# Kernel tuning notes

Hardware: AMD Instinct MI355X
Metric: run time of the kernel (lower is better)

The kernel has to match this reference:

```python
import jax, jax.numpy as jnp
import numpy as np

B, H, W = 32, 56, 56
C_IN, C_OUT, GROUPS, K = 256, 256, 32, 3
EPS = 1e-5


def setup_inputs() -> dict:
    key = jax.random.key(0)
    k1, k2 = jax.random.split(key, 2)
    x = jax.random.normal(k1, (B, H, W, C_IN), dtype=jnp.float32)
    # HWIO grouped-conv kernel: I = C_IN // GROUPS = 8; equivalent to the
    # concatenation of the 32 per-group [3,3,8,8] Conv2d kernels along O.
    w = jax.random.normal(k2, (K, K, C_IN // GROUPS, C_OUT), dtype=jnp.float32) * 0.05
    b = jnp.zeros((C_OUT,), dtype=jnp.float32)
    gamma = jnp.ones((C_OUT,), dtype=jnp.float32)
    beta = jnp.zeros((C_OUT,), dtype=jnp.float32)
    return {"x": x, "w": w, "b": b, "gamma": gamma, "beta": beta}


def reference(x, w, b, gamma, beta):
    # Grouped conv: same math as tf.split -> per-group Conv2d -> tf.concat,
    # expressed as one native grouped convolution (feature_group_count).
    y = jax.lax.conv_general_dilated(
        x, w,
        window_strides=(1, 1),
        padding="SAME",
        dimension_numbers=("NHWC", "HWIO", "NHWC"),
        feature_group_count=GROUPS,
    ) + b  # [B,H,W,C_OUT]
    # BatchNorm (training forward: batch statistics over N,H,W per channel)
    mean = jnp.mean(y, axis=(0, 1, 2))
    var = jnp.var(y, axis=(0, 1, 2))
    y = (y - mean) * jax.lax.rsqrt(var + EPS) * gamma + beta
    # Act('relu')
    return jax.nn.relu(y)
```

## Files before the change

kernel.cpp:

```cpp
#include <hip/hip_runtime.h>
#include <hip/hip_bf16.h>

#define BB 32
#define HH 56
#define WW 56
#define CC 256
#define NPIX (BB*HH*WW)
#define EPS 1e-5f

typedef short bf16x8 __attribute__((ext_vector_type(8)));
typedef float f32x4  __attribute__((ext_vector_type(4)));

__device__ __forceinline__ unsigned short f2bf(float f) {
    __hip_bfloat16 h = __float2bfloat16(f);
    return *reinterpret_cast<unsigned short*>(&h);
}


__global__ void k0_zero(float* stats) { stats[threadIdx.x] = 0.f; }

__global__ __launch_bounds__(256) void k1_conv(
    const float* __restrict__ x, const float* __restrict__ wgt,
    __hip_bfloat16* __restrict__ y, float* __restrict__ stats)
{
    __shared__ unsigned short xt[10*58*24];
    __shared__ unsigned short wb[16*160];
    __shared__ float bsum[16], bsq[16];

    const int gp = blockIdx.x;
    const int hb = blockIdx.y;
    const int b  = blockIdx.z;
    const int t  = threadIdx.x;
    const int h0 = hb * 8;

    if (t < 16) { bsum[t] = 0.f; bsq[t] = 0.f; }

    float4 v[10];
    int    off[10];
    #pragma unroll
    for (int j = 0; j < 10; ++j) {
        const int i   = j*256 + t;
        const int ci4 = i & 3;
        const int cq  = i >> 2;
        const int row = cq / 58;
        const int col = cq - row*58;
        const int hh  = h0 - 1 + row;
        const int wc  = col - 1;
        off[j] = (row*58 + col)*24 + ci4*4;
        v[j] = make_float4(0.f, 0.f, 0.f, 0.f);
        if (i < 2320 && (unsigned)hh < HH && (unsigned)wc < WW)
            v[j] = *(const float4*)(x + (((size_t)(b*HH + hh)*WW + wc)*CC + gp*16 + ci4*4));
    }
    {
        const int n  = t >> 4;
        const int k0 = t & 15;
        #pragma unroll
        for (int j = 0; j < 10; ++j) {
            const int kk  = k0 + j*16;
            const int g   = (kk >= 80);
            const int r   = kk - g*80;
            const int tap = r >> 3, ci = r & 7;
            unsigned short val = 0;
            if (tap < 9 && (n >> 3) == g)
                val = f2bf(wgt[(tap*8 + ci)*CC + gp*16 + n]);
            wb[n*160 + kk] = val;
        }
    }
    #pragma unroll
    for (int j = 0; j < 10; ++j) {
        if (j*256 + t < 2320) {
            ushort4 s;
            s.x = f2bf(v[j].x); s.y = f2bf(v[j].y);
            s.z = f2bf(v[j].z); s.w = f2bf(v[j].w);
            *(ushort4*)(xt + off[j]) = s;
        }
    }
    __syncthreads();

    const int lane = t & 63;
    const int rp   = t >> 6;
    const int n    = lane & 15;
    const int q    = lane >> 4;
    const int m    = lane & 15;
    const int rowr = rp*2 + (m >> 3);
    const int colb = m & 7;

    bf16x8 bfrag[5];
    #pragma unroll
    for (int s = 0; s < 5; ++s)
        bfrag[s] = *(const bf16x8*)(wb + n*160 + s*32 + q*8);

    int aoff[5];
    #pragma unroll
    for (int s = 0; s < 5; ++s) {
        int o  = s*4 + q;
        int g  = (o >= 10);
        int tp = o - g*10;
        if (tp == 9) tp = 0;
        int dh = tp / 3, dw = tp - dh*3;
        aoff[s] = ((rowr + dh)*58 + colb + dw)*24 + g*8;
    }

    const int hq = q >> 1;
    const int wq = (q & 1) * 4;
    float lsum = 0.f, lsq = 0.f;

    #pragma unroll 2
    for (int ct = 0; ct < 7; ++ct) {
        f32x4 acc = {0.f, 0.f, 0.f, 0.f};
        #pragma unroll
        for (int s = 0; s < 5; ++s) {
            bf16x8 af = *(const bf16x8*)(xt + aoff[s] + ct*192);
            acc = __builtin_amdgcn_mfma_f32_16x16x32_bf16(af, bfrag[s], acc, 0, 0, 0);
        }
        const int h = h0 + rp*2 + hq;
        const size_t base = (((size_t)(b*HH + h))*WW + ct*8 + wq)*CC + gp*16 + n;
        #pragma unroll
        for (int i = 0; i < 4; ++i) {
            float vv = acc[i];
            y[base + (size_t)i*CC] = __float2bfloat16(vv);
            lsum += vv;
            lsq  += vv * vv;
        }
    }

    atomicAdd(&bsum[n], lsum);
    atomicAdd(&bsq[n],  lsq);
    __syncthreads();
    if (t < 16) {
        atomicAdd(&stats[gp*16 + t],       bsum[t]);
        atomicAdd(&stats[256 + gp*16 + t], bsq[t]);
    }
}

__global__ void k2_finalize(const float* __restrict__ stats,
                            const float* __restrict__ gamma,
                            const float* __restrict__ beta,
                            float* __restrict__ ss)
{
    int c = threadIdx.x;
    float inv_n = 1.f / (float)NPIX;
    float mean = stats[c] * inv_n;
    float var  = stats[256 + c] * inv_n - mean * mean;
    float scale = gamma[c] * rsqrtf(var + EPS);
    ss[c]       = scale;
    ss[256 + c] = beta[c] - mean * scale;
}

__global__ __launch_bounds__(256) void k3_norm(
    const __hip_bfloat16* __restrict__ y, const float* __restrict__ ss,
    float* __restrict__ out)
{
    const int t   = threadIdx.x;
    const int oct = t & 31;
    const int pr  = t >> 5;
    const int c0  = oct * 8;

    float4 sc0 = *(const float4*)(ss + c0);
    float4 sc1 = *(const float4*)(ss + c0 + 4);
    float4 sh0 = *(const float4*)(ss + 256 + c0);
    float4 sh1 = *(const float4*)(ss + 256 + c0 + 4);

    const uint4* yv = (const uint4*)y;
    float4* ov = (float4*)out;
    const int px0 = blockIdx.x * 32 + pr;

    uint4 d[4];
    #pragma unroll
    for (int i = 0; i < 4; ++i)
        d[i] = yv[(size_t)(px0 + i*8)*32 + oct];

    #pragma unroll
    for (int i = 0; i < 4; ++i) {
        const int px = px0 + i*8;
        float f0 = __uint_as_float((d[i].x & 0xffffu) << 16);
        float f1 = __uint_as_float(d[i].x & 0xffff0000u);
        float f2 = __uint_as_float((d[i].y & 0xffffu) << 16);
        float f3 = __uint_as_float(d[i].y & 0xffff0000u);
        float f4 = __uint_as_float((d[i].z & 0xffffu) << 16);
        float f5 = __uint_as_float(d[i].z & 0xffff0000u);
        float f6 = __uint_as_float((d[i].w & 0xffffu) << 16);
        float f7 = __uint_as_float(d[i].w & 0xffff0000u);

        float4 o0, o1;
        o0.x = fmaxf(0.f, f0 * sc0.x + sh0.x);
        o0.y = fmaxf(0.f, f1 * sc0.y + sh0.y);
        o0.z = fmaxf(0.f, f2 * sc0.z + sh0.z);
        o0.w = fmaxf(0.f, f3 * sc0.w + sh0.w);
        o1.x = fmaxf(0.f, f4 * sc1.x + sh1.x);
        o1.y = fmaxf(0.f, f5 * sc1.y + sh1.y);
        o1.z = fmaxf(0.f, f6 * sc1.z + sh1.z);
        o1.w = fmaxf(0.f, f7 * sc1.w + sh1.w);

        ov[(size_t)px*64 + oct*2]     = o0;
        ov[(size_t)px*64 + oct*2 + 1] = o1;
    }
}

extern "C" void kernel_launch(void* const* d_in, const int* in_sizes, int n_in,
                              void* d_out, int out_size, void* d_ws, size_t ws_size,
                              hipStream_t stream) {
    const float* x     = (const float*)d_in[0];
    const float* wgt   = (const float*)d_in[1];
    const float* gamma = (const float*)d_in[3];
    const float* beta  = (const float*)d_in[4];
    float* out = (float*)d_out;

    float* stats = (float*)d_ws;
    float* ss    = (float*)((char*)d_ws + 2048);
    __hip_bfloat16* y = (__hip_bfloat16*)((char*)d_ws + 4096);

    k0_zero<<<1, 512, 0, stream>>>(stats);
    k1_conv<<<dim3(16, 7, BB), 256, 0, stream>>>(x, wgt, y, stats);
    k2_finalize<<<1, 256, 0, stream>>>(stats, gamma, beta, ss);
    k3_norm<<<NPIX/32, 256, 0, stream>>>(y, ss, out);
}
```

Measured before the change: 253.9 us.

## Swap MFMA operands for vectorized bf16 stores and load weights directly to registers

Swaps the A/B operands of the MFMA so each lane's accumulator holds 4 consecutive output channels for one pixel. This allows one 8-byte vector store of bf16 results instead of four scattered 2-byte stores. Weight fragments are now loaded directly from global memory into registers, which removes the shared weight buffer and its staging. Per-channel statistics are reduced with wavefront shuffles before a few LDS atomics, replacing per-lane LDS atomics, and launch bounds request 5 blocks per SM.

```diff
diff --git a/kernel.cpp b/kernel.cpp
--- a/kernel.cpp
+++ b/kernel.cpp
@@ -19,12 +19,11 @@
 
 __global__ void k0_zero(float* stats) { stats[threadIdx.x] = 0.f; }
 
-__global__ __launch_bounds__(256) void k1_conv(
+__global__ __launch_bounds__(256, 5) void k1_conv(
     const float* __restrict__ x, const float* __restrict__ wgt,
     __hip_bfloat16* __restrict__ y, float* __restrict__ stats)
 {
     __shared__ unsigned short xt[10*58*24];
-    __shared__ unsigned short wb[16*160];
     __shared__ float bsum[16], bsq[16];
 
     const int gp = blockIdx.x;
@@ -51,21 +50,6 @@
         if (i < 2320 && (unsigned)hh < HH && (unsigned)wc < WW)
             v[j] = *(const float4*)(x + (((size_t)(b*HH + hh)*WW + wc)*CC + gp*16 + ci4*4));
     }
-    {
-        const int n  = t >> 4;
-        const int k0 = t & 15;
-        #pragma unroll
-        for (int j = 0; j < 10; ++j) {
-            const int kk  = k0 + j*16;
-            const int g   = (kk >= 80);
-            const int r   = kk - g*80;
-            const int tap = r >> 3, ci = r & 7;
-            unsigned short val = 0;
-            if (tap < 9 && (n >> 3) == g)
-                val = f2bf(wgt[(tap*8 + ci)*CC + gp*16 + n]);
-            wb[n*160 + kk] = val;
-        }
-    }
     #pragma unroll
     for (int j = 0; j < 10; ++j) {
         if (j*256 + t < 2320) {
@@ -75,20 +59,32 @@
             *(ushort4*)(xt + off[j]) = s;
         }
     }
-    __syncthreads();
 
     const int lane = t & 63;
     const int rp   = t >> 6;
     const int n    = lane & 15;
     const int q    = lane >> 4;
+
+    bf16x8 wfrag[5];
+    #pragma unroll
+    for (int s = 0; s < 5; ++s) {
+        const int o   = s*4 + q;
+        const int g   = (o >= 10);
+        const int tap = o - g*10;
+        bf16x8 f = {0,0,0,0,0,0,0,0};
+        if (tap < 9 && (n >> 3) == g) {
+            #pragma unroll
+            for (int e = 0; e < 8; ++e)
+                f[e] = (short)f2bf(wgt[(tap*8 + e)*CC + gp*16 + n]);
+        }
+        wfrag[s] = f;
+    }
+
+    __syncthreads();
+
     const int m    = lane & 15;
     const int rowr = rp*2 + (m >> 3);
     const int colb = m & 7;
-
-    bf16x8 bfrag[5];
-    #pragma unroll
-    for (int s = 0; s < 5; ++s)
-        bfrag[s] = *(const bf16x8*)(wb + n*160 + s*32 + q*8);
 
     int aoff[5];
     #pragma unroll
@@ -101,9 +97,10 @@
         aoff[s] = ((rowr + dh)*58 + colb + dw)*24 + g*8;
     }
 
-    const int hq = q >> 1;
-    const int wq = (q & 1) * 4;
-    float lsum = 0.f, lsq = 0.f;
+    const int h = h0 + rowr;
+    const size_t pixbase = ((size_t)(b*HH + h))*WW;
+    float lsum[4] = {0.f, 0.f, 0.f, 0.f};
+    float lsq[4]  = {0.f, 0.f, 0.f, 0.f};
 
     #pragma unroll 2
     for (int ct = 0; ct < 7; ++ct) {
@@ -111,21 +108,34 @@
         #pragma unroll
         for (int s = 0; s < 5; ++s) {
             bf16x8 af = *(const bf16x8*)(xt + aoff[s] + ct*192);
-            acc = __builtin_amdgcn_mfma_f32_16x16x32_bf16(af, bfrag[s], acc, 0, 0, 0);
-        }
-        const int h = h0 + rp*2 + hq;
-        const size_t base = (((size_t)(b*HH + h))*WW + ct*8 + wq)*CC + gp*16 + n;
+            acc = __builtin_amdgcn_mfma_f32_16x16x32_bf16(wfrag[s], af, acc, 0, 0, 0);
+        }
+        ushort4 st;
+        st.x = f2bf(acc[0]); st.y = f2bf(acc[1]);
+        st.z = f2bf(acc[2]); st.w = f2bf(acc[3]);
+        *(ushort4*)(y + (pixbase + ct*8 + colb)*CC + gp*16 + q*4) = st;
         #pragma unroll
         for (int i = 0; i < 4; ++i) {
-            float vv = acc[i];
-            y[base + (size_t)i*CC] = __float2bfloat16(vv);
-            lsum += vv;
-            lsq  += vv * vv;
-        }
-    }
-
-    atomicAdd(&bsum[n], lsum);
-    atomicAdd(&bsq[n],  lsq);
+            lsum[i] += acc[i];
+            lsq[i]  += acc[i]*acc[i];
+        }
+    }
+
+    #pragma unroll
+    for (int d = 8; d >= 1; d >>= 1) {
+        #pragma unroll
+        for (int i = 0; i < 4; ++i) {
+            lsum[i] += __shfl_xor(lsum[i], d);
+            lsq[i]  += __shfl_xor(lsq[i],  d);
+        }
+    }
+    if (m == 0) {
+        #pragma unroll
+        for (int i = 0; i < 4; ++i) {
+            atomicAdd(&bsum[q*4 + i], lsum[i]);
+            atomicAdd(&bsq[q*4 + i],  lsq[i]);
+        }
+    }
     __syncthreads();
     if (t < 16) {
         atomicAdd(&stats[gp*16 + t],       bsum[t]);
```

Result: faster. 247.2 us (-2.6%).
